# Performance work log

Hardware: AMD Instinct MI355X
Metric: run time of the kernel (lower is better)

Reference implementation:

```python
import jax, jax.numpy as jnp
import numpy as np

B, C, D, H, W = 4, 128, 16, 16, 16
C8 = C // 8
TEXT = 256
N = D * H * W


def setup_inputs() -> dict:
    key = jax.random.key(0)
    ks = jax.random.split(key, 13)
    s = lambda fan: 1.0 / np.sqrt(fan)
    return {
        "x": jax.random.normal(ks[0], (B, C, D, H, W), jnp.float32),
        "text_emb": jax.random.normal(ks[1], (B, TEXT), jnp.float32),
        "Wq": jax.random.normal(ks[2], (C8, C), jnp.float32) * s(C),
        "bq": jax.random.normal(ks[3], (C8,), jnp.float32) * 0.01,
        "Wk": jax.random.normal(ks[4], (C8, C), jnp.float32) * s(C),
        "bk": jax.random.normal(ks[5], (C8,), jnp.float32) * 0.01,
        "Wv": jax.random.normal(ks[6], (C, C), jnp.float32) * s(C),
        "bv": jax.random.normal(ks[7], (C,), jnp.float32) * 0.01,
        "Wtk": jax.random.normal(ks[8], (C8, TEXT), jnp.float32) * s(TEXT),
        "btk": jax.random.normal(ks[9], (C8,), jnp.float32) * 0.01,
        "Wtv": jax.random.normal(ks[10], (C, TEXT), jnp.float32) * s(TEXT),
        "btv": jax.random.normal(ks[11], (C,), jnp.float32) * 0.01,
        # gamma is zero-init in the original; use a nonzero value so the
        # attention path contributes to the output (and to gradients).
        "gamma": jax.random.normal(ks[12], (1,), jnp.float32) * 0.1 + 0.5,
    }


def reference(x, text_emb, Wq, bq, Wk, bk, Wv, bv, Wtk, btk, Wtv, btv, gamma):
    b, c, d, h, w = x.shape
    n = d * h * w
    xf = x.reshape(b, c, n)                       # [B, C, N]
    # 1x1x1 convs == channel matmuls
    q = jnp.einsum('oc,bcn->bno', Wq, xf) + bq    # [B, N, C8]
    k = jnp.einsum('oc,bcn->bon', Wk, xf) + bk[None, :, None]  # [B, C8, N]
    v = jnp.einsum('oc,bcn->bon', Wv, xf) + bv[None, :, None]  # [B, C, N]
    # text-conditioned additive key/value (broadcast over all voxels)
    tk = (text_emb @ Wtk.T + btk)[:, :, None]     # [B, C8, 1]
    tv = (text_emb @ Wtv.T + btv)[:, :, None]     # [B, C, 1]
    k = k + tk
    v = v + tv
    # unscaled attention: softmax over keys
    scores = jnp.einsum('bno,bom->bnm', q, k)     # [B, N, N]
    attn = jax.nn.softmax(scores, axis=-1)
    # out[b,c,n] = sum_m v[b,c,m] * attn[b,n,m]
    out = jnp.einsum('bcm,bnm->bcn', v, attn).reshape(b, c, d, h, w)
    return gamma * out + x
```

## Files before the change

### kernel.cpp

```cpp
#include <hip/hip_runtime.h>
#include <math.h>

#define BB 4
#define CC 128
#define C8 16
#define TEXTN 256
#define NN 4096
#define WQB 32
#define NT 32

typedef __attribute__((ext_vector_type(8))) __bf16 bf16x8;
typedef __attribute__((ext_vector_type(16))) float f32x16;

#define LOG2E 1.44269504088896340736f

static __device__ __forceinline__ ushort f2bf(float f) {
  unsigned u = __builtin_bit_cast(unsigned, f);
  u += 0x7FFFu + ((u >> 16) & 1u);
  return (ushort)(u >> 16);
}

static __device__ __forceinline__ float exp2a(float x) {
#if __has_builtin(__builtin_amdgcn_exp2f)
  return __builtin_amdgcn_exp2f(x);
#else
  return exp2f(x);
#endif
}

static __device__ __forceinline__ unsigned cvt_pk_bf16(float lo, float hi) {
  unsigned r;
  asm("v_cvt_pk_bf16_f32 %0, %1, %2" : "=v"(r) : "v"(lo), "v"(hi));
  return r;
}
static __device__ __forceinline__ void pl32swap(unsigned &a, unsigned &b) {
  asm("v_permlane32_swap_b32 %0, %1" : "+v"(a), "+v"(b));
}

__global__ __launch_bounds__(256) void k_text(
    const float* __restrict__ text, const float* __restrict__ Wtk,
    const float* __restrict__ btk, const float* __restrict__ Wtv,
    const float* __restrict__ btv, float* __restrict__ tkv) {
  __shared__ float ts[TEXTN];
  int b = blockIdx.x;
  for (int i = threadIdx.x; i < TEXTN; i += 256) ts[i] = text[b * TEXTN + i];
  __syncthreads();
  int o = threadIdx.x;
  if (o < 144) {
    const float* w;
    float acc;
    if (o < 16) { w = Wtk + o * TEXTN; acc = btk[o]; }
    else        { w = Wtv + (o - 16) * TEXTN; acc = btv[o - 16]; }
    #pragma unroll 8
    for (int t = 0; t < TEXTN; t++) acc += w[t] * ts[t];
    tkv[b * 144 + o] = acc;
  }
}

__global__ __launch_bounds__(320) void k_qkv(
    const float* __restrict__ x,
    const float* __restrict__ Wq, const float* __restrict__ bq,
    const float* __restrict__ Wk, const float* __restrict__ bk,
    const float* __restrict__ Wv, const float* __restrict__ bv,
    const float* __restrict__ tkv,
    ushort* __restrict__ qt, ushort* __restrict__ kt, ushort* __restrict__ vtB) {
  __shared__ __align__(16) ushort xs[64 * 128];
  int b = blockIdx.x >> 6;
  int n0 = (blockIdx.x & 63) * 64;
  int t = threadIdx.x;
  int w = t >> 6, lane = t & 63, l31 = lane & 31, hi = lane >> 5;

  for (int i = t; i < 1024; i += 320) {
    int n = i & 63, ch = i >> 6;
    union { ushort u[8]; uint4 v; } pk;
    #pragma unroll
    for (int j = 0; j < 8; ++j)
      pk.u[j] = f2bf(x[((size_t)b * CC + ch * 8 + j) * NN + n0 + n]);
    *(uint4*)&xs[n * 128 + ((ch ^ (n & 15)) << 3)] = pk.v;
  }

  const float* wrow;
  if (w == 0) wrow = (l31 < 16) ? (Wq + l31 * CC) : (Wk + (l31 - 16) * CC);
  else        wrow = Wv + (size_t)(32 * (w - 1) + l31) * CC;
  bf16x8 af[8];
  #pragma unroll
  for (int ks = 0; ks < 8; ++ks) {
    float4 u0 = *(const float4*)&wrow[ks * 16 + hi * 8];
    float4 u1 = *(const float4*)&wrow[ks * 16 + hi * 8 + 4];
    union { ushort u[8]; bf16x8 v; } tmp;
    tmp.u[0] = f2bf(u0.x); tmp.u[1] = f2bf(u0.y); tmp.u[2] = f2bf(u0.z); tmp.u[3] = f2bf(u0.w);
    tmp.u[4] = f2bf(u1.x); tmp.u[5] = f2bf(u1.y); tmp.u[6] = f2bf(u1.z); tmp.u[7] = f2bf(u1.w);
    af[ks] = tmp.v;
  }
  float badd[16];
  #pragma unroll
  for (int r = 0; r < 16; ++r) {
    int ol = (r & 3) + 8 * (r >> 2) + 4 * hi;
    if (w == 0) badd[r] = (ol < 16) ? bq[ol] : (bk[ol - 16] + tkv[b * 144 + ol - 16]);
    else { int c = 32 * (w - 1) + ol; badd[r] = bv[c] + tkv[b * 144 + 16 + c]; }
  }
  __syncthreads();

  #pragma unroll
  for (int n32 = 0; n32 < 2; ++n32) {
    int n = n32 * 32 + l31;
    int ng = n0 + n;
    bf16x8 bf[8];
    #pragma unroll
    for (int ks = 0; ks < 8; ++ks)
      bf[ks] = *(const bf16x8*)&xs[n * 128 + (((ks * 2 + hi) ^ (n & 15)) << 3)];
    f32x16 d;
    #pragma unroll
    for (int r = 0; r < 16; ++r) d[r] = 0.f;
    #pragma unroll
    for (int ks = 0; ks < 8; ++ks)
      d = __builtin_amdgcn_mfma_f32_32x32x16_bf16(af[ks], bf[ks], d, 0, 0, 0);
    #pragma unroll
    for (int g = 0; g < 4; ++g) {
      int o0 = 8 * g + 4 * hi;
      float v0 = d[g * 4 + 0] + badd[g * 4 + 0];
      float v1 = d[g * 4 + 1] + badd[g * 4 + 1];
      float v2 = d[g * 4 + 2] + badd[g * 4 + 2];
      float v3 = d[g * 4 + 3] + badd[g * 4 + 3];
      if (w == 0 && o0 < 16) { v0 *= LOG2E; v1 *= LOG2E; v2 *= LOG2E; v3 *= LOG2E; }
      ushort4 pkv;
      pkv.x = f2bf(v0); pkv.y = f2bf(v1); pkv.z = f2bf(v2); pkv.w = f2bf(v3);
      if (w == 0) {
        if (o0 < 16) *(ushort4*)&qt[(b * NN + ng) * C8 + o0] = pkv;
        else         *(ushort4*)&kt[(b * NN + ng) * C8 + o0 - 16] = pkv;
      } else {
        int c0 = 32 * (w - 1) + o0;
        int base = b * (NN / 8) * CC * 8 + (ng >> 3) * (CC * 8) + (ng & 7);
        vtB[base + (c0 + 0) * 8] = pkv.x;
        vtB[base + (c0 + 1) * 8] = pkv.y;
        vtB[base + (c0 + 2) * 8] = pkv.z;
        vtB[base + (c0 + 3) * 8] = pkv.w;
      }
    }
  }
}

__global__ __launch_bounds__(512, 4) void k_attn(
    const ushort* __restrict__ qt, const ushort* __restrict__ kt,
    const ushort* __restrict__ vtB, const float* __restrict__ x,
    const float* __restrict__ gamma_p, float* __restrict__ out) {
  __shared__ __align__(16) float mergeAcc[4][2][1024];
  __shared__ float mergeL[4][2][32];
  __shared__ float invGL[32];

  int b = blockIdx.x >> 7;
  int q0 = (blockIdx.x & 127) * WQB;
  int t = threadIdx.x;
  int w = t >> 6, lane = t & 63, l31 = lane & 31, hi = lane >> 5;
  int ms = w & 3, ch = w >> 2;

  const ushort* ktb = kt + (size_t)b * NN * C8;
  const ushort* vbb = vtB + (size_t)b * (NN / 8) * CC * 8;

  bf16x8 qf = *(const bf16x8*)&qt[((size_t)b * NN + q0 + l31) * C8 + hi * 8];

  f32x16 acc0, acc1;
  #pragma unroll
  for (int r = 0; r < 16; ++r) { acc0[r] = 0.f; acc1[r] = 0.f; }
  float lp = 0.f;

  const ushort* kp  = ktb + (ms * 32 + l31) * C8 + hi * 8;
  const ushort* vp0 = vbb + (size_t)(ms * 4 + 0 + hi) * (CC * 8) + (ch * 64 + l31) * 8;
  const ushort* vp1 = vbb + (size_t)(ms * 4 + 2 + hi) * (CC * 8) + (ch * 64 + l31) * 8;

  bf16x8 kfA, kfB;
  kfA = *(const bf16x8*)kp; kp += 128 * C8;

#define STEP(CK, NK)                                                          \
  {                                                                           \
    NK = *(const bf16x8*)kp; kp += 128 * C8;                                  \
    bf16x8 vA0 = *(const bf16x8*)(vp0);                   \
    bf16x8 vA1 = *(const bf16x8*)(vp0 + 256);             \
    bf16x8 vB0 = *(const bf16x8*)(vp1);                   \
    bf16x8 vB1 = *(const bf16x8*)(vp1 + 256);             \
    vp0 += 16 * CC * 8; vp1 += 16 * CC * 8;                                   \
    f32x16 z;                                                                 \
    _Pragma("unroll")                                                         \
    for (int r = 0; r < 16; ++r) z[r] = 0.f;                                  \
    f32x16 s = __builtin_amdgcn_mfma_f32_32x32x16_bf16(CK, qf, z, 0, 0, 0);   \
    float p[16];                                                              \
    _Pragma("unroll")                                                         \
    for (int r = 0; r < 16; ++r) p[r] = exp2a(s[r]);                          \
    float y0 = p[0] + p[1],   y1 = p[2] + p[3];                               \
    float y2 = p[4] + p[5],   y3 = p[6] + p[7];                               \
    float y4 = p[8] + p[9],   y5 = p[10] + p[11];                             \
    float y6 = p[12] + p[13], y7 = p[14] + p[15];                             \
    y0 += y1; y2 += y3; y4 += y5; y6 += y7;                                   \
    lp += (y0 + y2) + (y4 + y6);                                              \
    bf16x8 pf0, pf1;                                                          \
    {                                                                         \
      unsigned a0 = cvt_pk_bf16(p[0], p[1]), b0 = cvt_pk_bf16(p[4], p[5]);    \
      unsigned c0 = cvt_pk_bf16(p[2], p[3]), d0 = cvt_pk_bf16(p[6], p[7]);    \
      pl32swap(a0, b0); pl32swap(c0, d0);                                     \
      union { unsigned u[4]; bf16x8 v; } u0; u0.u[0] = a0; u0.u[1] = c0;      \
      u0.u[2] = b0; u0.u[3] = d0; pf0 = u0.v;                                 \
      unsigned a1 = cvt_pk_bf16(p[8], p[9]), b1 = cvt_pk_bf16(p[12], p[13]);  \
      unsigned c1 = cvt_pk_bf16(p[10], p[11]), d1 = cvt_pk_bf16(p[14], p[15]);\
      pl32swap(a1, b1); pl32swap(c1, d1);                                     \
      union { unsigned u[4]; bf16x8 v; } u1; u1.u[0] = a1; u1.u[1] = c1;      \
      u1.u[2] = b1; u1.u[3] = d1; pf1 = u1.v;                                 \
    }                                                                         \
    __builtin_amdgcn_s_setprio(1);                                            \
    acc0 = __builtin_amdgcn_mfma_f32_32x32x16_bf16(vA0, pf0, acc0, 0, 0, 0);  \
    acc1 = __builtin_amdgcn_mfma_f32_32x32x16_bf16(vA1, pf0, acc1, 0, 0, 0);  \
    acc0 = __builtin_amdgcn_mfma_f32_32x32x16_bf16(vB0, pf1, acc0, 0, 0, 0);  \
    acc1 = __builtin_amdgcn_mfma_f32_32x32x16_bf16(vB1, pf1, acc1, 0, 0, 0);  \
    __builtin_amdgcn_s_setprio(0);                                            \
  }

  for (int tt = 0; tt < NT; tt += 2) {
    STEP(kfA, kfB)
    STEP(kfB, kfA)
  }
#undef STEP

  if (ch == 0) mergeL[ms][hi][l31] = lp;
  __syncthreads();
  if (t < 32) {
    float L = 0.f;
    #pragma unroll
    for (int m2 = 0; m2 < 4; ++m2)
      #pragma unroll
      for (int h2 = 0; h2 < 2; ++h2) L += mergeL[m2][h2][t];
    invGL[t] = gamma_p[0] / L;
  }

  #pragma unroll
  for (int ph = 0; ph < 2; ++ph) {
    if (ph) __syncthreads();
    {
      const f32x16& A = ph ? acc1 : acc0;
      #pragma unroll
      for (int r = 0; r < 16; ++r)
        mergeAcc[ms][ch][((r & 3) + 8 * (r >> 2) + 4 * hi) * 32 + l31] = A[r];
    }
    __syncthreads();
    int idx = t * 4;
    int qq = idx & 31, cl = idx >> 5;
    int chh = cl >> 5, crow = cl & 31;
    float4 sum = *(const float4*)&mergeAcc[0][chh][crow * 32 + qq];
    #pragma unroll
    for (int m2 = 1; m2 < 4; ++m2) {
      float4 sv = *(const float4*)&mergeAcc[m2][chh][crow * 32 + qq];
      sum.x += sv.x; sum.y += sv.y; sum.z += sv.z; sum.w += sv.w;
    }
    float4 gl = *(const float4*)&invGL[qq];
    int c = chh * 64 + ph * 32 + crow;
    size_t base = ((size_t)b * CC + c) * NN + q0 + qq;
    float4 xv = *(const float4*)&x[base];
    float4 ov;
    ov.x = sum.x * gl.x + xv.x;
    ov.y = sum.y * gl.y + xv.y;
    ov.z = sum.z * gl.z + xv.z;
    ov.w = sum.w * gl.w + xv.w;
    *(float4*)&out[base] = ov;
  }
}

extern "C" void kernel_launch(void* const* d_in, const int* in_sizes, int n_in,
                              void* d_out, int out_size, void* d_ws, size_t ws_size,
                              hipStream_t stream) {
  const float* x     = (const float*)d_in[0];
  const float* text  = (const float*)d_in[1];
  const float* Wq    = (const float*)d_in[2];
  const float* bq    = (const float*)d_in[3];
  const float* Wk    = (const float*)d_in[4];
  const float* bk    = (const float*)d_in[5];
  const float* Wv    = (const float*)d_in[6];
  const float* bv    = (const float*)d_in[7];
  const float* Wtk   = (const float*)d_in[8];
  const float* btk   = (const float*)d_in[9];
  const float* Wtv   = (const float*)d_in[10];
  const float* btv   = (const float*)d_in[11];
  const float* gamma = (const float*)d_in[12];
  float* outp = (float*)d_out;

  char* wsb = (char*)d_ws;
  float*  tkv = (float*)wsb;
  ushort* qt  = (ushort*)(wsb + 4096);
  ushort* kt  = (ushort*)(wsb + 4096 + 524288);
  ushort* vtB = (ushort*)(wsb + 4096 + 2 * 524288);

  k_text<<<BB, 256, 0, stream>>>(text, Wtk, btk, Wtv, btv, tkv);
  k_qkv<<<BB * NN / 64, 320, 0, stream>>>(x, Wq, bq, Wk, bk, Wv, bv, tkv, qt, kt, vtB);
  k_attn<<<BB * NN / WQB, 512, 0, stream>>>(qt, kt, vtB, x, gamma, outp);
}
```

Measured before the change: 55.63 us.

## Process 64 queries per attention block to reuse K/V fragments across two tiles

Each attention block now covers 64 queries as two 32-query MFMA tiles, so every K and V fragment loaded from memory feeds twice as many MFMAs. Accumulators, row-sum tracking and the epilogue merge are doubled to match, and the wave-to-(key slice, channel half) mapping is rearranged. The aim is to halve K/V load traffic per query. In exchange the grid is halved, register pressure roughly doubles, and the occupancy hint in the launch bounds is dropped, which may leave fewer waves to hide latency.

New measurement: 52.89 us. 1.05x faster.

```diff
diff --git a/kernel.cpp b/kernel.cpp
--- a/kernel.cpp
+++ b/kernel.cpp
@@ -6,7 +6,7 @@
 #define C8 16
 #define TEXTN 256
 #define NN 4096
-#define WQB 32
+#define WQB 64
 #define NT 32
 
 typedef __attribute__((ext_vector_type(8))) __bf16 bf16x8;
@@ -140,29 +140,34 @@
   }
 }
 
-__global__ __launch_bounds__(512, 4) void k_attn(
+__global__ __launch_bounds__(512) void k_attn(
     const ushort* __restrict__ qt, const ushort* __restrict__ kt,
     const ushort* __restrict__ vtB, const float* __restrict__ x,
     const float* __restrict__ gamma_p, float* __restrict__ out) {
   __shared__ __align__(16) float mergeAcc[4][2][1024];
-  __shared__ float mergeL[4][2][32];
-  __shared__ float invGL[32];
-
-  int b = blockIdx.x >> 7;
-  int q0 = (blockIdx.x & 127) * WQB;
+  __shared__ float mergeL[4][2][2][32];
+  __shared__ float invGL[64];
+
+  int b = blockIdx.x >> 6;
+  int q0 = (blockIdx.x & 63) * WQB;
   int t = threadIdx.x;
   int w = t >> 6, lane = t & 63, l31 = lane & 31, hi = lane >> 5;
-  int ms = w & 3, ch = w >> 2;
+  int ms = w >> 1, ch = w & 1;
 
   const ushort* ktb = kt + (size_t)b * NN * C8;
   const ushort* vbb = vtB + (size_t)b * (NN / 8) * CC * 8;
 
-  bf16x8 qf = *(const bf16x8*)&qt[((size_t)b * NN + q0 + l31) * C8 + hi * 8];
-
-  f32x16 acc0, acc1;
-  #pragma unroll
-  for (int r = 0; r < 16; ++r) { acc0[r] = 0.f; acc1[r] = 0.f; }
-  float lp = 0.f;
+  bf16x8 qfA = *(const bf16x8*)&qt[((size_t)b * NN + q0 + l31) * C8 + hi * 8];
+  bf16x8 qfB = *(const bf16x8*)&qt[((size_t)b * NN + q0 + 32 + l31) * C8 + hi * 8];
+
+  f32x16 accA0, accA1, accB0, accB1;
+  #pragma unroll
+  for (int r = 0; r < 16; ++r) { accA0[r] = 0.f; accA1[r] = 0.f; accB0[r] = 0.f; accB1[r] = 0.f; }
+  float lpA = 0.f, lpB = 0.f;
+
+  f32x16 z;
+  #pragma unroll
+  for (int r = 0; r < 16; ++r) z[r] = 0.f;
 
   const ushort* kp  = ktb + (ms * 32 + l31) * C8 + hi * 8;
   const ushort* vp0 = vbb + (size_t)(ms * 4 + 0 + hi) * (CC * 8) + (ch * 64 + l31) * 8;
@@ -170,6 +175,20 @@
 
   bf16x8 kfA, kfB;
   kfA = *(const bf16x8*)kp; kp += 128 * C8;
+
+#define MKPF(P, OUT0, OUT1)                                                   \
+  {                                                                           \
+    unsigned a0 = cvt_pk_bf16(P[0], P[1]), b0 = cvt_pk_bf16(P[4], P[5]);      \
+    unsigned c0 = cvt_pk_bf16(P[2], P[3]), d0 = cvt_pk_bf16(P[6], P[7]);      \
+    pl32swap(a0, b0); pl32swap(c0, d0);                                       \
+    union { unsigned u[4]; bf16x8 v; } u0; u0.u[0] = a0; u0.u[1] = c0;        \
+    u0.u[2] = b0; u0.u[3] = d0; OUT0 = u0.v;                                  \
+    unsigned a1 = cvt_pk_bf16(P[8], P[9]), b1 = cvt_pk_bf16(P[12], P[13]);    \
+    unsigned c1 = cvt_pk_bf16(P[10], P[11]), d1 = cvt_pk_bf16(P[14], P[15]);  \
+    pl32swap(a1, b1); pl32swap(c1, d1);                                       \
+    union { unsigned u[4]; bf16x8 v; } u1; u1.u[0] = a1; u1.u[1] = c1;        \
+    u1.u[2] = b1; u1.u[3] = d1; OUT1 = u1.v;                                  \
+  }
 
 #define STEP(CK, NK)                                                          \
   {                                                                           \
@@ -179,37 +198,37 @@
     bf16x8 vB0 = *(const bf16x8*)(vp1);                   \
     bf16x8 vB1 = *(const bf16x8*)(vp1 + 256);             \
     vp0 += 16 * CC * 8; vp1 += 16 * CC * 8;                                   \
-    f32x16 z;                                                                 \
+    f32x16 sA = __builtin_amdgcn_mfma_f32_32x32x16_bf16(CK, qfA, z, 0, 0, 0); \
+    f32x16 sB = __builtin_amdgcn_mfma_f32_32x32x16_bf16(CK, qfB, z, 0, 0, 0); \
+    float pA[16], pB[16];                                                     \
     _Pragma("unroll")                                                         \
-    for (int r = 0; r < 16; ++r) z[r] = 0.f;                                  \
-    f32x16 s = __builtin_amdgcn_mfma_f32_32x32x16_bf16(CK, qf, z, 0, 0, 0);   \
-    float p[16];                                                              \
+    for (int r = 0; r < 16; ++r) pA[r] = exp2a(sA[r]);                        \
     _Pragma("unroll")                                                         \
-    for (int r = 0; r < 16; ++r) p[r] = exp2a(s[r]);                          \
-    float y0 = p[0] + p[1],   y1 = p[2] + p[3];                               \
-    float y2 = p[4] + p[5],   y3 = p[6] + p[7];                               \
-    float y4 = p[8] + p[9],   y5 = p[10] + p[11];                             \
-    float y6 = p[12] + p[13], y7 = p[14] + p[15];                             \
-    y0 += y1; y2 += y3; y4 += y5; y6 += y7;                                   \
-    lp += (y0 + y2) + (y4 + y6);                                              \
-    bf16x8 pf0, pf1;                                                          \
+    for (int r = 0; r < 16; ++r) pB[r] = exp2a(sB[r]);                        \
     {                                                                         \
-      unsigned a0 = cvt_pk_bf16(p[0], p[1]), b0 = cvt_pk_bf16(p[4], p[5]);    \
-      unsigned c0 = cvt_pk_bf16(p[2], p[3]), d0 = cvt_pk_bf16(p[6], p[7]);    \
-      pl32swap(a0, b0); pl32swap(c0, d0);                                     \
-      union { unsigned u[4]; bf16x8 v; } u0; u0.u[0] = a0; u0.u[1] = c0;      \
-      u0.u[2] = b0; u0.u[3] = d0; pf0 = u0.v;                                 \
-      unsigned a1 = cvt_pk_bf16(p[8], p[9]), b1 = cvt_pk_bf16(p[12], p[13]);  \
-      unsigned c1 = cvt_pk_bf16(p[10], p[11]), d1 = cvt_pk_bf16(p[14], p[15]);\
-      pl32swap(a1, b1); pl32swap(c1, d1);                                     \
-      union { unsigned u[4]; bf16x8 v; } u1; u1.u[0] = a1; u1.u[1] = c1;      \
-      u1.u[2] = b1; u1.u[3] = d1; pf1 = u1.v;                                 \
+      float y0 = (pA[0] + pA[1]) + (pA[2] + pA[3]);                           \
+      float y1 = (pA[4] + pA[5]) + (pA[6] + pA[7]);                           \
+      float y2 = (pA[8] + pA[9]) + (pA[10] + pA[11]);                         \
+      float y3 = (pA[12] + pA[13]) + (pA[14] + pA[15]);                       \
+      lpA += (y0 + y1) + (y2 + y3);                                           \
+      float u0 = (pB[0] + pB[1]) + (pB[2] + pB[3]);                           \
+      float u1 = (pB[4] + pB[5]) + (pB[6] + pB[7]);                           \
+      float u2 = (pB[8] + pB[9]) + (pB[10] + pB[11]);                         \
+      float u3 = (pB[12] + pB[13]) + (pB[14] + pB[15]);                       \
+      lpB += (u0 + u1) + (u2 + u3);                                           \
     }                                                                         \
+    bf16x8 pfA0, pfA1, pfB0, pfB1;                                            \
+    MKPF(pA, pfA0, pfA1)                                                      \
+    MKPF(pB, pfB0, pfB1)                                                      \
     __builtin_amdgcn_s_setprio(1);                                            \
-    acc0 = __builtin_amdgcn_mfma_f32_32x32x16_bf16(vA0, pf0, acc0, 0, 0, 0);  \
-    acc1 = __builtin_amdgcn_mfma_f32_32x32x16_bf16(vA1, pf0, acc1, 0, 0, 0);  \
-    acc0 = __builtin_amdgcn_mfma_f32_32x32x16_bf16(vB0, pf1, acc0, 0, 0, 0);  \
-    acc1 = __builtin_amdgcn_mfma_f32_32x32x16_bf16(vB1, pf1, acc1, 0, 0, 0);  \
+    accA0 = __builtin_amdgcn_mfma_f32_32x32x16_bf16(vA0, pfA0, accA0, 0, 0, 0); \
+    accA1 = __builtin_amdgcn_mfma_f32_32x32x16_bf16(vA1, pfA0, accA1, 0, 0, 0); \
+    accB0 = __builtin_amdgcn_mfma_f32_32x32x16_bf16(vA0, pfB0, accB0, 0, 0, 0); \
+    accB1 = __builtin_amdgcn_mfma_f32_32x32x16_bf16(vA1, pfB0, accB1, 0, 0, 0); \
+    accA0 = __builtin_amdgcn_mfma_f32_32x32x16_bf16(vB0, pfA1, accA0, 0, 0, 0); \
+    accA1 = __builtin_amdgcn_mfma_f32_32x32x16_bf16(vB1, pfA1, accA1, 0, 0, 0); \
+    accB0 = __builtin_amdgcn_mfma_f32_32x32x16_bf16(vB0, pfB1, accB0, 0, 0, 0); \
+    accB1 = __builtin_amdgcn_mfma_f32_32x32x16_bf16(vB1, pfB1, accB1, 0, 0, 0); \
     __builtin_amdgcn_s_setprio(0);                                            \
   }
 
@@ -218,48 +237,55 @@
     STEP(kfB, kfA)
   }
 #undef STEP
-
-  if (ch == 0) mergeL[ms][hi][l31] = lp;
+#undef MKPF
+
+  if (ch == 0) {
+    mergeL[ms][hi][0][l31] = lpA;
+    mergeL[ms][hi][1][l31] = lpB;
+  }
   __syncthreads();
-  if (t < 32) {
+  if (t < 64) {
     float L = 0.f;
     #pragma unroll
     for (int m2 = 0; m2 < 4; ++m2)
       #pragma unroll
-      for (int h2 = 0; h2 < 2; ++h2) L += mergeL[m2][h2][t];
+      for (int h2 = 0; h2 < 2; ++h2) L += mergeL[m2][h2][t >> 5][t & 31];
     invGL[t] = gamma_p[0] / L;
   }
 
-  #pragma unroll
-  for (int ph = 0; ph < 2; ++ph) {
-    if (ph) __syncthreads();
-    {
-      const f32x16& A = ph ? acc1 : acc0;
-      #pragma unroll
-      for (int r = 0; r < 16; ++r)
-        mergeAcc[ms][ch][((r & 3) + 8 * (r >> 2) + 4 * hi) * 32 + l31] = A[r];
-    }
-    __syncthreads();
-    int idx = t * 4;
-    int qq = idx & 31, cl = idx >> 5;
-    int chh = cl >> 5, crow = cl & 31;
-    float4 sum = *(const float4*)&mergeAcc[0][chh][crow * 32 + qq];
-    #pragma unroll
-    for (int m2 = 1; m2 < 4; ++m2) {
-      float4 sv = *(const float4*)&mergeAcc[m2][chh][crow * 32 + qq];
-      sum.x += sv.x; sum.y += sv.y; sum.z += sv.z; sum.w += sv.w;
-    }
-    float4 gl = *(const float4*)&invGL[qq];
-    int c = chh * 64 + ph * 32 + crow;
-    size_t base = ((size_t)b * CC + c) * NN + q0 + qq;
-    float4 xv = *(const float4*)&x[base];
-    float4 ov;
-    ov.x = sum.x * gl.x + xv.x;
-    ov.y = sum.y * gl.y + xv.y;
-    ov.z = sum.z * gl.z + xv.z;
-    ov.w = sum.w * gl.w + xv.w;
-    *(float4*)&out[base] = ov;
-  }
+#define EPI(ACC, QT, CB, FIRST)                                               \
+  {                                                                           \
+    if (!(FIRST)) __syncthreads();                                            \
+    _Pragma("unroll")                                                         \
+    for (int r = 0; r < 16; ++r)                                              \
+      mergeAcc[ms][ch][(((r & 3) + 8 * (r >> 2) + 4 * hi) << 5) | l31] = ACC[r]; \
+    __syncthreads();                                                          \
+    int idx = t * 4;                                                          \
+    int qq = idx & 31, cl = idx >> 5;                                         \
+    int chh = cl >> 5, crow = cl & 31;                                        \
+    float4 sum = *(const float4*)&mergeAcc[0][chh][crow * 32 + qq];           \
+    _Pragma("unroll")                                                         \
+    for (int m2 = 1; m2 < 4; ++m2) {                                          \
+      float4 sv = *(const float4*)&mergeAcc[m2][chh][crow * 32 + qq];         \
+      sum.x += sv.x; sum.y += sv.y; sum.z += sv.z; sum.w += sv.w;             \
+    }                                                                         \
+    float4 gl = *(const float4*)&invGL[(QT) * 32 + qq];                       \
+    int c = chh * 64 + (CB) * 32 + crow;                                      \
+    size_t base = ((size_t)b * CC + c) * NN + q0 + (QT) * 32 + qq;            \
+    float4 xv = *(const float4*)&x[base];                                     \
+    float4 ov;                                                                \
+    ov.x = sum.x * gl.x + xv.x;                                               \
+    ov.y = sum.y * gl.y + xv.y;                                               \
+    ov.z = sum.z * gl.z + xv.z;                                               \
+    ov.w = sum.w * gl.w + xv.w;                                               \
+    *(float4*)&out[base] = ov;                                                \
+  }
+
+  EPI(accA0, 0, 0, 1)
+  EPI(accA1, 0, 1, 0)
+  EPI(accB0, 1, 0, 0)
+  EPI(accB1, 1, 1, 0)
+#undef EPI
 }
 
 extern "C" void kernel_launch(void* const* d_in, const int* in_sizes, int n_in,
```
